# Optimization experiments

Measured on AMD Instinct MI355X. Metric: run time of the kernel, lower is better.

The kernel has to match this reference:

```python
import jax, jax.numpy as jnp
import numpy as np

# DH-SFNN: 2 dendritic LIF layers (denri, no tanh, reset-by-subtraction) + leaky readout integrator.
GAMMA = 0.5   # surrogate gradient scale
LENS = 0.5    # surrogate gradient width
VTH = 1.0     # spike threshold
DT = 1.0

@jax.custom_vjp
def spike_fn(x):
    # Heaviside forward, Gaussian surrogate backward (act_fun_adp)
    return (x > 0.0).astype(x.dtype)

def _spike_fwd(x):
    return spike_fn(x), x

def _spike_bwd(x, g):
    sg = GAMMA * jnp.exp(-x * x / (2.0 * LENS * LENS)) / (jnp.sqrt(2.0 * jnp.pi) * LENS)
    return (g * sg,)

spike_fn.defvjp(_spike_fwd, _spike_bwd)

B, T, IN, H, O, K = 256, 250, 700, 256, 20, 4  # batch, time, in_dim, hidden, out_dim, branch
WARMUP = 10


def _branch_mask(rng, out_dim, in_dim, k):
    # Each neuron's k branches see a disjoint random partition of the inputs.
    m = np.zeros((out_dim * k, in_dim), np.float32)
    step = in_dim // k
    for i in range(out_dim):
        perm = rng.permutation(in_dim)
        for j in range(k):
            m[i * k + j, perm[j * step:(j + 1) * step]] = 1.0
    return m


def setup_inputs() -> dict:
    key = jax.random.key(0)
    ks = jax.random.split(key, 12)
    rng = np.random.default_rng(0)
    s1 = 1.0 / np.sqrt(IN)
    s2 = 1.0 / np.sqrt(H)
    # branch-masked dense weights (apply_mask() already baked in)
    W1 = jax.random.uniform(ks[0], (H * K, IN), minval=-s1, maxval=s1) * jnp.asarray(_branch_mask(rng, H, IN, K))
    b1 = jax.random.uniform(ks[1], (H * K,), minval=-s1, maxval=s1)
    tau_n1 = jax.random.uniform(ks[2], (H, K), minval=2.0, maxval=6.0)
    tau_m1 = jax.random.uniform(ks[3], (H,), minval=0.0, maxval=4.0)
    W2 = jax.random.uniform(ks[4], (H * K, H), minval=-s2, maxval=s2) * jnp.asarray(_branch_mask(rng, H, H, K))
    b2 = jax.random.uniform(ks[5], (H * K,), minval=-s2, maxval=s2)
    tau_n2 = jax.random.uniform(ks[6], (H, K), minval=2.0, maxval=6.0)
    tau_m2 = jax.random.uniform(ks[7], (H,), minval=0.0, maxval=4.0)
    Wr = jax.random.uniform(ks[8], (O, H), minval=-s2, maxval=s2)
    br = jax.random.uniform(ks[9], (O,), minval=-s2, maxval=s2)
    tau_mr = jax.random.uniform(ks[10], (O,), minval=0.0, maxval=4.0)
    # sparse binary spike train input (SHD-like)
    x = (jax.random.uniform(ks[11], (B, T, IN)) < 0.1).astype(jnp.float32)
    return dict(x=x, W1=W1, b1=b1, tau_n1=tau_n1, tau_m1=tau_m1,
                W2=W2, b2=b2, tau_n2=tau_n2, tau_m2=tau_m2,
                Wr=Wr, br=br, tau_mr=tau_mr, warmup=WARMUP)


def reference(x, W1, b1, tau_n1, tau_m1, W2, b2, tau_n2, tau_m2, Wr, br, tau_mr, warmup):
    Bb, Tt, _ = x.shape
    beta1 = jax.nn.sigmoid(tau_n1)   # [H,K] dendritic decay
    alpha1 = jax.nn.sigmoid(tau_m1)  # [H]   soma decay
    beta2 = jax.nn.sigmoid(tau_n2)
    alpha2 = jax.nn.sigmoid(tau_m2)
    alphar = jax.nn.sigmoid(tau_mr)  # [O]

    def dense_branch(inp, W, b):
        return (inp @ W.T + b).reshape(inp.shape[0], -1, K)  # [B,H,K]

    def step(carry, xt):
        d1, m1, s1, d2, m2, s2, mr, acc, t = carry
        # layer 1: dendritic filtering then LIF with soft reset
        d1 = beta1 * d1 + (1.0 - beta1) * dense_branch(xt, W1, b1)
        m1 = m1 * alpha1 + (1.0 - alpha1) * DT * d1.sum(-1) - VTH * s1
        s1 = spike_fn(m1 - VTH)
        # layer 2
        d2 = beta2 * d2 + (1.0 - beta2) * dense_branch(s1, W2, b2)
        m2 = m2 * alpha2 + (1.0 - alpha2) * DT * d2.sum(-1) - VTH * s2
        s2 = spike_fn(m2 - VTH)
        # leaky readout integrator
        mr = mr * alphar + (1.0 - alphar) * (s2 @ Wr.T + br)
        acc = acc + jnp.where(t >= warmup, mr, jnp.zeros_like(mr))
        return (d1, m1, s1, d2, m2, s2, mr, acc, t + 1), None

    z = lambda *s: jnp.zeros(s, x.dtype)
    carry0 = (z(Bb, H, K), z(Bb, H), z(Bb, H),
              z(Bb, H, K), z(Bb, H), z(Bb, H),
              z(Bb, O), z(Bb, O), jnp.int32(0))
    carry, _ = jax.lax.scan(step, carry0, jnp.moveaxis(x, 1, 0))
    acc = carry[7]
    return acc / (Tt - warmup)  # readout_mode == 'mean'
```

## Files before the change

kernel.cpp:

```cpp
#include <hip/hip_runtime.h>
#include <hip/hip_bf16.h>

typedef unsigned short us16;
typedef unsigned int u32;

#define B_   256
#define T_   250
#define IN_  700
#define KP_  704
#define H_   256
#define O_   20
#define HK_  1024
#define NPAIR_ (B_ * T_)
#define LDP_ 40
#define CP_  136

typedef __attribute__((ext_vector_type(8))) short short8;
typedef __attribute__((ext_vector_type(4))) float f32x4;

__device__ __forceinline__ float bfbits(unsigned int lo16) {
    union { unsigned int i; float f; } v; v.i = lo16 << 16; return v.f;
}
__device__ __forceinline__ float bflo(unsigned int u) {
    union { unsigned int i; float f; } v; v.i = u << 16; return v.f;
}
__device__ __forceinline__ float bfhi(unsigned int u) {
    union { unsigned int i; float f; } v; v.i = u & 0xffff0000u; return v.f;
}
__device__ __forceinline__ us16 f2bfu(float f) {
    __hip_bfloat16 h = __float2bfloat16(f);
    union { __hip_bfloat16 h; us16 u; } c; c.h = h; return c.u;
}
__device__ __forceinline__ float sigm(float x) { return 1.0f / (1.0f + expf(-x)); }
__device__ __forceinline__ int rfl(int v) { return __builtin_amdgcn_readfirstlane(v); }

__device__ __forceinline__ bool detect_bf16(const us16* __restrict__ taun) {
    int ok = 0;
#pragma unroll
    for (int i = 0; i < 8; i += 2) ok += ((taun[i] >> 8) == 0x40) ? 1 : 0;
    return ok == 4;
}
__device__ __forceinline__ float ldany(const void* __restrict__ p, long i, bool isb) {
    return isb ? bfbits(((const us16*)p)[i]) : ((const float*)p)[i];
}

__device__ __forceinline__ void async_cp16(const us16* g, us16* l) {
    __builtin_amdgcn_global_load_lds(
        (const __attribute__((address_space(1))) u32*)g,
        (__attribute__((address_space(3))) u32*)l, 16, 0, 0);
}

__global__ __launch_bounds__(256) void cvt_rows2(
    const void* __restrict__ xin, const void* __restrict__ w1in,
    us16* __restrict__ xout, us16* __restrict__ w1out,
    const us16* __restrict__ taun) {
    const bool isb = detect_bf16(taun);
    const int r = blockIdx.x * 4 + (threadIdx.x >> 6);
    const int l = threadIdx.x & 63;
    const void* in; us16* out; long ibase, obase;
    if (r < NPAIR_) {
        in = xin;  out = xout;  ibase = (long)r * IN_; obase = (long)r * KP_;
    } else {
        const int r2 = r - NPAIR_;
        if (r2 >= HK_) return;
        in = w1in; out = w1out; ibase = (long)r2 * IN_; obase = (long)r2 * KP_;
    }
    for (int c = l; c < 88; c += 64) {
        uint4 o;
        if (c < 87) {
            if (isb) {
                uint2 lo = *(const uint2*)((const us16*)in + ibase + 8 * c);
                uint2 hi = *(const uint2*)((const us16*)in + ibase + 8 * c + 4);
                o.x = lo.x; o.y = lo.y; o.z = hi.x; o.w = hi.y;
            } else {
                float4 f0 = *(const float4*)((const float*)in + ibase + 8 * c);
                float4 f1 = *(const float4*)((const float*)in + ibase + 8 * c + 4);
                o.x = (u32)f2bfu(f0.x) | ((u32)f2bfu(f0.y) << 16);
                o.y = (u32)f2bfu(f0.z) | ((u32)f2bfu(f0.w) << 16);
                o.z = (u32)f2bfu(f1.x) | ((u32)f2bfu(f1.y) << 16);
                o.w = (u32)f2bfu(f1.z) | ((u32)f2bfu(f1.w) << 16);
            }
        } else {
            o.z = 0u; o.w = 0u;
            if (isb) {
                uint2 lo = *(const uint2*)((const us16*)in + ibase + 696);
                o.x = lo.x; o.y = lo.y;
            } else {
                float4 f0 = *(const float4*)((const float*)in + ibase + 696);
                o.x = (u32)f2bfu(f0.x) | ((u32)f2bfu(f0.y) << 16);
                o.y = (u32)f2bfu(f0.z) | ((u32)f2bfu(f0.w) << 16);
            }
        }
        *(uint4*)(out + obase + 8 * c) = o;
    }
}

__global__ void transpose_to_bf16(const void* __restrict__ in, us16* __restrict__ out,
                                  int R, int C, const us16* __restrict__ taun) {
    const bool isb = detect_bf16(taun);
    __shared__ us16 tile[32][33];
    int c0 = blockIdx.x * 32, r0 = blockIdx.y * 32;
    int tx = threadIdx.x, ty = threadIdx.y;
#pragma unroll
    for (int j = 0; j < 32; j += 8) {
        int r = r0 + ty + j, c = c0 + tx;
        if (r < R && c < C) tile[ty + j][tx] = f2bfu(ldany(in, (long)r * C + c, isb));
    }
    __syncthreads();
#pragma unroll
    for (int j = 0; j < 32; j += 8) {
        int c = c0 + ty + j, r = r0 + tx;
        if (c < C && r < R) out[(long)c * R + r] = tile[tx][ty + j];
    }
}

__global__ __launch_bounds__(256) void gemm_bf(
    const us16* __restrict__ Xb, const us16* __restrict__ W1b,
    us16* __restrict__ Apre)
{
    __shared__ __align__(16) us16 smem[32768];

    const int L  = blockIdx.x;
    const int mt = (L & 7) + ((L >> 6) << 3);
    const int nt = (L >> 3) & 7;
    if (mt >= NPAIR_ / 128) return;
    const int m0 = mt * 128, n0 = nt * 128;

    const int tid  = threadIdx.x;
    const int lane = tid & 63;
    const int w    = tid >> 6;
    const int wr   = w >> 1, wc = w & 1;
    const int l16  = lane & 15, quad = lane >> 4;

    const int rr    = lane >> 3;
    const int ccsw  = ((lane & 7) ^ rr) * 8;
    const us16* xg[4]; const us16* wg[4];
    int asl[4], bsl[4];
#pragma unroll
    for (int i = 0; i < 4; ++i) {
        const int blkrow = (w * 4 + i) * 8;
        xg[i]  = Xb  + (long)(m0 + blkrow + rr) * KP_ + ccsw;
        wg[i]  = W1b + (long)(n0 + blkrow + rr) * KP_ + ccsw;
        asl[i] = (w * 4 + i) * 512;
        bsl[i] = 8192 + (w * 4 + i) * 512;
    }

    f32x4 acc[4][4];
#pragma unroll
    for (int i = 0; i < 4; ++i)
#pragma unroll
        for (int j = 0; j < 4; ++j) acc[i][j] = (f32x4){0.f, 0.f, 0.f, 0.f};

    const int sw = l16 & 7;
    int aoff0[4], aoff1[4], boff0[4], boff1[4];
#pragma unroll
    for (int i = 0; i < 4; ++i) {
        const int ar = wr * 64 + i * 16 + l16;
        const int br = wc * 64 + i * 16 + l16;
        aoff0[i] = ar * 64 + ((quad ^ sw) << 3);
        aoff1[i] = ar * 64 + (((quad + 4) ^ sw) << 3);
        boff0[i] = 8192 + br * 64 + ((quad ^ sw) << 3);
        boff1[i] = 8192 + br * 64 + (((quad + 4) ^ sw) << 3);
    }

#pragma unroll
    for (int i = 0; i < 4; ++i) async_cp16(xg[i], smem + asl[i]);
#pragma unroll
    for (int i = 0; i < 4; ++i) async_cp16(wg[i], smem + bsl[i]);
    __syncthreads();

    for (int s = 0; s < 11; ++s) {
        const int cur = (s & 1) * 16384;
        const int nxt = 16384 - cur;
        if (s + 1 < 11) {
            const int kb = (s + 1) * 64;
#pragma unroll
            for (int i = 0; i < 4; ++i) async_cp16(xg[i] + kb, smem + nxt + asl[i]);
#pragma unroll
            for (int i = 0; i < 4; ++i) async_cp16(wg[i] + kb, smem + nxt + bsl[i]);
        }

        short8 af[4][2], bfv[4][2];
#pragma unroll
        for (int i = 0; i < 4; ++i) {
            af[i][0]  = *(const short8*)(smem + cur + aoff0[i]);
            af[i][1]  = *(const short8*)(smem + cur + aoff1[i]);
            bfv[i][0] = *(const short8*)(smem + cur + boff0[i]);
            bfv[i][1] = *(const short8*)(smem + cur + boff1[i]);
        }
#pragma unroll
        for (int h = 0; h < 2; ++h)
#pragma unroll
            for (int i = 0; i < 4; ++i)
#pragma unroll
                for (int j = 0; j < 4; ++j)
                    acc[i][j] = __builtin_amdgcn_mfma_f32_16x16x32_bf16(
                        af[i][h], bfv[j][h], acc[i][j], 0, 0, 0);

        __syncthreads();
    }

#pragma unroll
    for (int i = 0; i < 4; ++i)
#pragma unroll
        for (int j = 0; j < 4; ++j)
#pragma unroll
            for (int r = 0; r < 4; ++r)
                smem[(wr * 64 + i * 16 + quad * 4 + r) * CP_ +
                     (wc * 64 + j * 16 + l16)] = f2bfu(acc[i][j][r]);
    __syncthreads();
    {
        const int c8 = (lane & 15) * 8;
#pragma unroll
        for (int r2 = 0; r2 < 8; ++r2) {
            const int row = w * 32 + r2 * 4 + (lane >> 4);
            const uint4 v = *(const uint4*)(smem + row * CP_ + c8);
            *(uint4*)(Apre + (long)(m0 + row) * HK_ + n0 + c8) = v;
        }
    }
}

__global__ __launch_bounds__(64) void dhsfnn_wave2(
    const us16* __restrict__ Apre,
    const void* __restrict__ b1,  const void* __restrict__ tau_n1,
    const void* __restrict__ tau_m1,
    const void* __restrict__ b2,  const void* __restrict__ tau_n2,
    const void* __restrict__ tau_m2,
    const void* __restrict__ Wr,  const void* __restrict__ br,
    const void* __restrict__ tau_mr,
    const us16* __restrict__ W2T,
    const int* __restrict__ warmup_p,
    void* __restrict__ out)
{
    __shared__ __align__(16) us16 ring[2][16 * HK_];

    const int lane = threadIdx.x;
    const int b    = blockIdx.x;
    const bool isb = detect_bf16((const us16*)tau_n1);
    const int wu   = *warmup_p;

    const us16* apb = Apre + (long)b * T_ * HK_;

    for (int seg = 0; seg < 32; ++seg)
        async_cp16(apb + seg * 512 + lane * 8, ring[0] + seg * 512);

    float be1[16], cb1[16], ce1[16], be2[16], cb2[16], ce2[16], d1[16], d2[16];
#pragma unroll
    for (int e = 0; e < 16; ++e) {
        const long gi = (e < 8) ? ((long)lane * 8 + e) : (512 + (long)lane * 8 + e - 8);
        const float t1 = sigm(ldany(tau_n1, gi, isb));
        be1[e] = t1; ce1[e] = 1.f - t1; cb1[e] = ce1[e] * ldany(b1, gi, isb);
        const float t2 = sigm(ldany(tau_n2, gi, isb));
        be2[e] = t2; ce2[e] = 1.f - t2; cb2[e] = ce2[e] * ldany(b2, gi, isb);
        d1[e] = 0.f; d2[e] = 0.f;
    }
    float al1[4], cal1[4], al2[4], cal2[4], m1[4], s1[4], m2[4], s2[4];
#pragma unroll
    for (int j = 0; j < 4; ++j) {
        const int n = (j < 2) ? (2 * lane + j) : (128 + 2 * lane + (j - 2));
        al1[j] = sigm(ldany(tau_m1, n, isb)); cal1[j] = 1.f - al1[j];
        al2[j] = sigm(ldany(tau_m2, n, isb)); cal2[j] = 1.f - al2[j];
        m1[j] = 0.f; s1[j] = 0.f; m2[j] = 0.f; s2[j] = 0.f;
    }
    float alr = 0.f, brv = 0.f;
    if (lane < O_) { alr = sigm(ldany(tau_mr, lane, isb)); brv = ldany(br, lane, isb); }
    float mrv = 0.f, accO = 0.f;

    for (int c = 0; c < 16; ++c) {
        asm volatile("s_waitcnt vmcnt(0)" ::: "memory");

        if (c + 1 < 16) {
            const int t1c  = (c + 1) * 16;
            const int nseg = ((T_ - t1c < 16) ? (T_ - t1c) : 16) * 2;
            const us16* src = apb + (long)t1c * HK_;
            us16* dst = ring[(c + 1) & 1];
            for (int seg = 0; seg < nseg; ++seg)
                async_cp16(src + seg * 512 + lane * 8, dst + seg * 512);
        }

        const int t0 = c * 16;
        const int nst = (T_ - t0 < 16) ? (T_ - t0) : 16;
        const us16* rb = ring[c & 1];
        uint4 cLo = *(const uint4*)(rb + lane * 8);
        uint4 cHi = *(const uint4*)(rb + 512 + lane * 8);
        for (int q = 0; q < nst; ++q) {
            uint4 nLo = cLo, nHi = cHi;
            if (q + 1 < nst) {
                nLo = *(const uint4*)(rb + (q + 1) * HK_ + lane * 8);
                nHi = *(const uint4*)(rb + (q + 1) * HK_ + 512 + lane * 8);
            }
            const int t = t0 + q;
            float a[16];
            a[0]=bflo(cLo.x);  a[1]=bfhi(cLo.x);  a[2]=bflo(cLo.y);  a[3]=bfhi(cLo.y);
            a[4]=bflo(cLo.z);  a[5]=bfhi(cLo.z);  a[6]=bflo(cLo.w);  a[7]=bfhi(cLo.w);
            a[8]=bflo(cHi.x);  a[9]=bfhi(cHi.x);  a[10]=bflo(cHi.y); a[11]=bfhi(cHi.y);
            a[12]=bflo(cHi.z); a[13]=bfhi(cHi.z); a[14]=bflo(cHi.w); a[15]=bfhi(cHi.w);

#pragma unroll
            for (int e = 0; e < 16; ++e)
                d1[e] = be1[e] * d1[e] + cb1[e] + ce1[e] * a[e];

            unsigned long long bal1[4];
#pragma unroll
            for (int j = 0; j < 4; ++j) {
                const float s = (d1[j*4+0] + d1[j*4+1]) + (d1[j*4+2] + d1[j*4+3]);
                m1[j] = m1[j] * al1[j] + cal1[j] * s - s1[j];
                s1[j] = (m1[j] > 1.0f) ? 1.f : 0.f;
                bal1[j] = __ballot(s1[j] > 0.f);
            }

            if ((bal1[0] | bal1[1] | bal1[2] | bal1[3]) != 0ull) {
                float g[16];
#pragma unroll
                for (int e = 0; e < 16; ++e) g[e] = 0.f;
                for (int j2 = 0; j2 < 4; ++j2) {
                    unsigned long long mm = bal1[j2];
                    while (mm) {
                        const int i = __ffsll(mm) - 1; mm &= mm - 1;
                        const int n = (j2 < 2) ? (2 * i + j2) : (128 + 2 * i + (j2 - 2));
                        const us16* wv = W2T + ((long)n << 10);
                        const uint4 wl = *(const uint4*)(wv + lane * 8);
                        const uint4 wh = *(const uint4*)(wv + 512 + lane * 8);
                        g[0]+=bflo(wl.x);  g[1]+=bfhi(wl.x);  g[2]+=bflo(wl.y);  g[3]+=bfhi(wl.y);
                        g[4]+=bflo(wl.z);  g[5]+=bfhi(wl.z);  g[6]+=bflo(wl.w);  g[7]+=bfhi(wl.w);
                        g[8]+=bflo(wh.x);  g[9]+=bfhi(wh.x);  g[10]+=bflo(wh.y); g[11]+=bfhi(wh.y);
                        g[12]+=bflo(wh.z); g[13]+=bfhi(wh.z); g[14]+=bflo(wh.w); g[15]+=bfhi(wh.w);
                    }
                }
#pragma unroll
                for (int e = 0; e < 16; ++e)
                    d2[e] = be2[e] * d2[e] + cb2[e] + ce2[e] * g[e];
            } else {
#pragma unroll
                for (int e = 0; e < 16; ++e)
                    d2[e] = be2[e] * d2[e] + cb2[e];
            }

            unsigned long long bal2[4];
#pragma unroll
            for (int j = 0; j < 4; ++j) {
                const float s = (d2[j*4+0] + d2[j*4+1]) + (d2[j*4+2] + d2[j*4+3]);
                m2[j] = m2[j] * al2[j] + cal2[j] * s - s2[j];
                s2[j] = (m2[j] > 1.0f) ? 1.f : 0.f;
                bal2[j] = __ballot(s2[j] > 0.f);
            }

            if (lane < O_) {
                float sum = brv;
                if ((bal2[0] | bal2[1] | bal2[2] | bal2[3]) != 0ull) {
                    for (int j2 = 0; j2 < 4; ++j2) {
                        unsigned long long mm = bal2[j2];
                        while (mm) {
                            const int i = __ffsll(mm) - 1; mm &= mm - 1;
                            const int n = (j2 < 2) ? (2 * i + j2) : (128 + 2 * i + (j2 - 2));
                            sum += ldany(Wr, (long)lane * H_ + n, isb);
                        }
                    }
                }
                mrv = alr * mrv + (1.f - alr) * sum;
                if (t >= wu) accO += mrv;
            }
            cLo = nLo; cHi = nHi;
        }
    }

    if (lane < O_) {
        const float res = accO / (float)(T_ - wu);
        if (isb) ((us16*)out)[b * O_ + lane] = f2bfu(res);
        else     ((float*)out)[b * O_ + lane] = res;
    }
}

#define GA_LOAD(S, AV, BV) do {                                               \
    const int k0_ = (S) * 32 + half16;                                        \
    if (k0_ + 16 <= IN_) {                                                    \
        if (isb) {                                                            \
            const us16* pa_ = (const us16*)X  + arow + k0_;                   \
            const us16* pb_ = (const us16*)W1 + brow + k0_;                   \
            uint2 a0_ = *(const uint2*)pa_,        a1_ = *(const uint2*)(pa_ + 4);  \
            uint2 a2_ = *(const uint2*)(pa_ + 8),  a3_ = *(const uint2*)(pa_ + 12); \
            uint2 b0_ = *(const uint2*)pb_,        b1_ = *(const uint2*)(pb_ + 4);  \
            uint2 b2_ = *(const uint2*)(pb_ + 8),  b3_ = *(const uint2*)(pb_ + 12); \
            AV[0]=a0_.x; AV[1]=a0_.y; AV[2]=a1_.x; AV[3]=a1_.y;               \
            AV[4]=a2_.x; AV[5]=a2_.y; AV[6]=a3_.x; AV[7]=a3_.y;               \
            BV[0]=b0_.x; BV[1]=b0_.y; BV[2]=b1_.x; BV[3]=b1_.y;               \
            BV[4]=b2_.x; BV[5]=b2_.y; BV[6]=b3_.x; BV[7]=b3_.y;               \
        } else {                                                              \
            const float* pa_ = (const float*)X  + arow + k0_;                 \
            const float* pb_ = (const float*)W1 + brow + k0_;                 \
            float4 fa0_ = *(const float4*)pa_,        fa1_ = *(const float4*)(pa_ + 4);  \
            float4 fa2_ = *(const float4*)(pa_ + 8),  fa3_ = *(const float4*)(pa_ + 12); \
            float4 fb0_ = *(const float4*)pb_,        fb1_ = *(const float4*)(pb_ + 4);  \
            float4 fb2_ = *(const float4*)(pb_ + 8),  fb3_ = *(const float4*)(pb_ + 12); \
            AV[0] = (unsigned)f2bfu(fa0_.x) | ((unsigned)f2bfu(fa0_.y) << 16); \
            AV[1] = (unsigned)f2bfu(fa0_.z) | ((unsigned)f2bfu(fa0_.w) << 16); \
            AV[2] = (unsigned)f2bfu(fa1_.x) | ((unsigned)f2bfu(fa1_.y) << 16); \
            AV[3] = (unsigned)f2bfu(fa1_.z) | ((unsigned)f2bfu(fa1_.w) << 16); \
            AV[4] = (unsigned)f2bfu(fa2_.x) | ((unsigned)f2bfu(fa2_.y) << 16); \
            AV[5] = (unsigned)f2bfu(fa2_.z) | ((unsigned)f2bfu(fa2_.w) << 16); \
            AV[6] = (unsigned)f2bfu(fa3_.x) | ((unsigned)f2bfu(fa3_.y) << 16); \
            AV[7] = (unsigned)f2bfu(fa3_.z) | ((unsigned)f2bfu(fa3_.w) << 16); \
            BV[0] = (unsigned)f2bfu(fb0_.x) | ((unsigned)f2bfu(fb0_.y) << 16); \
            BV[1] = (unsigned)f2bfu(fb0_.z) | ((unsigned)f2bfu(fb0_.w) << 16); \
            BV[2] = (unsigned)f2bfu(fb1_.x) | ((unsigned)f2bfu(fb1_.y) << 16); \
            BV[3] = (unsigned)f2bfu(fb1_.z) | ((unsigned)f2bfu(fb1_.w) << 16); \
            BV[4] = (unsigned)f2bfu(fb2_.x) | ((unsigned)f2bfu(fb2_.y) << 16); \
            BV[5] = (unsigned)f2bfu(fb2_.z) | ((unsigned)f2bfu(fb2_.w) << 16); \
            BV[6] = (unsigned)f2bfu(fb3_.x) | ((unsigned)f2bfu(fb3_.y) << 16); \
            BV[7] = (unsigned)f2bfu(fb3_.z) | ((unsigned)f2bfu(fb3_.w) << 16); \
        }                                                                     \
    } else {                                                                  \
        _Pragma("unroll")                                                     \
        for (int e_ = 0; e_ < 8; ++e_) { AV[e_] = 0u; BV[e_] = 0u; }          \
        _Pragma("unroll")                                                     \
        for (int e_ = 0; e_ < 16; ++e_) {                                     \
            int k_ = k0_ + e_;                                                \
            if (k_ < IN_) {                                                   \
                unsigned va_ = (unsigned)f2bfu(ldany(X,  arow + k_, isb));    \
                unsigned vb_ = (unsigned)f2bfu(ldany(W1, brow + k_, isb));    \
                AV[e_ >> 1] |= va_ << ((e_ & 1) * 16);                        \
                BV[e_ >> 1] |= vb_ << ((e_ & 1) * 16);                        \
            }                                                                 \
        }                                                                     \
    }                                                                         \
} while (0)

#define GA_STORE(AV, BV) do {                                                 \
    uint4 u0_; u0_.x = AV[0]; u0_.y = AV[1]; u0_.z = AV[2]; u0_.w = AV[3];    \
    uint4 u1_; u1_.x = AV[4]; u1_.y = AV[5]; u1_.z = AV[6]; u1_.w = AV[7];    \
    uint4 v0_; v0_.x = BV[0]; v0_.y = BV[1]; v0_.z = BV[2]; v0_.w = BV[3];    \
    uint4 v1_; v1_.x = BV[4]; v1_.y = BV[5]; v1_.z = BV[6]; v1_.w = BV[7];    \
    *(uint4*)asw       = u0_; *(uint4*)(asw + 8) = u1_;                       \
    *(uint4*)bsw       = v0_; *(uint4*)(bsw + 8) = v1_;                       \
} while (0)

#define GA_MFMA() do {                                                        \
    short8 af_[4], bf_[4];                                                    \
    _Pragma("unroll")                                                         \
    for (int i_ = 0; i_ < 4; ++i_) af_[i_] = *(const short8*)(As + aoff[i_]); \
    _Pragma("unroll")                                                         \
    for (int j_ = 0; j_ < 4; ++j_) bf_[j_] = *(const short8*)(Bs + boff[j_]); \
    _Pragma("unroll")                                                         \
    for (int i_ = 0; i_ < 4; ++i_)                                            \
        _Pragma("unroll")                                                     \
        for (int j_ = 0; j_ < 4; ++j_)                                        \
            acc[i_][j_] = __builtin_amdgcn_mfma_f32_16x16x32_bf16(            \
                af_[i_], bf_[j_], acc[i_][j_], 0, 0, 0);                      \
} while (0)

__global__ __launch_bounds__(256) void gemm_apre(
    const void* __restrict__ X, const void* __restrict__ W1,
    const us16* __restrict__ taun, us16* __restrict__ Apre)
{
    const bool isb = detect_bf16(taun);
    __shared__ __align__(16) us16 As[128 * LDP_];
    __shared__ __align__(16) us16 Bs[128 * LDP_];

    const int L  = blockIdx.x;
    const int mt = (L & 7) + ((L >> 6) << 3);
    const int nt = (L >> 3) & 7;
    if (mt >= NPAIR_ / 128) return;
    const int m0 = mt * 128, n0 = nt * 128;

    const int tid  = threadIdx.x;
    const int lane = tid & 63;
    const int w    = tid >> 6;
    const int wr   = w >> 1, wc = w & 1;
    const int l16  = lane & 15, quad = lane >> 4;
    const int ra   = tid >> 1;
    const int half16 = (tid & 1) * 16;

    f32x4 acc[4][4];
#pragma unroll
    for (int i = 0; i < 4; ++i)
#pragma unroll
        for (int j = 0; j < 4; ++j) acc[i][j] = (f32x4){0.f, 0.f, 0.f, 0.f};

    int aoff[4], boff[4];
#pragma unroll
    for (int i = 0; i < 4; ++i) {
        aoff[i] = (wr * 64 + i * 16 + l16) * LDP_ + quad * 8;
        boff[i] = (wc * 64 + i * 16 + l16) * LDP_ + quad * 8;
    }

    const long arow = (long)(m0 + ra) * IN_;
    const long brow = (long)(n0 + ra) * IN_;
    us16* asw = As + ra * LDP_ + half16;
    us16* bsw = Bs + ra * LDP_ + half16;

    unsigned av0[8], bv0[8], av1[8], bv1[8];
    GA_LOAD(0, av0, bv0);

    for (int ss = 0; ss < 11; ++ss) {
        __syncthreads();
        GA_STORE(av0, bv0);
        __syncthreads();
        GA_LOAD(2 * ss + 1, av1, bv1);
        GA_MFMA();
        __syncthreads();
        GA_STORE(av1, bv1);
        __syncthreads();
        if (ss < 10) GA_LOAD(2 * ss + 2, av0, bv0);
        GA_MFMA();
    }

#pragma unroll
    for (int i = 0; i < 4; ++i) {
#pragma unroll
        for (int j = 0; j < 4; ++j) {
            const int gm = m0 + wr * 64 + i * 16 + quad * 4;
            const int gn = n0 + wc * 64 + j * 16 + l16;
            us16* op = Apre + (long)gm * HK_ + gn;
#pragma unroll
            for (int r = 0; r < 4; ++r)
                op[(long)r * HK_] = f2bfu(acc[i][j][r]);
        }
    }
}

__global__ __launch_bounds__(64) void dhsfnn_wave(
    const us16* __restrict__ Apre,
    const void* __restrict__ b1,  const void* __restrict__ tau_n1,
    const void* __restrict__ tau_m1,
    const void* __restrict__ b2,  const void* __restrict__ tau_n2,
    const void* __restrict__ tau_m2,
    const void* __restrict__ Wr,  const void* __restrict__ br,
    const void* __restrict__ tau_mr,
    const us16* __restrict__ W2T,
    const int* __restrict__ warmup_p,
    void* __restrict__ out)
{
    const int lane = threadIdx.x;
    const int b    = blockIdx.x;
    const bool isb = detect_bf16((const us16*)tau_n1);
    const int wu   = *warmup_p;

    float be1[16], cb1[16], be2[16], cb2[16], d1[16], d2[16];
#pragma unroll
    for (int e = 0; e < 16; ++e) {
        const long gi = (long)lane * 16 + e;
        const float t1 = sigm(ldany(tau_n1, gi, isb));
        be1[e] = t1; cb1[e] = (1.f - t1) * ldany(b1, gi, isb);
        const float t2 = sigm(ldany(tau_n2, gi, isb));
        be2[e] = t2; cb2[e] = (1.f - t2) * ldany(b2, gi, isb);
        d1[e] = 0.f; d2[e] = 0.f;
    }
    float al1[4], al2[4], m1[4], s1[4], m2[4], s2[4];
#pragma unroll
    for (int j = 0; j < 4; ++j) {
        al1[j] = sigm(ldany(tau_m1, lane * 4 + j, isb));
        al2[j] = sigm(ldany(tau_m2, lane * 4 + j, isb));
        m1[j] = 0.f; s1[j] = 0.f; m2[j] = 0.f; s2[j] = 0.f;
    }
    float alr = 0.f, brv = 0.f;
    if (lane < O_) { alr = sigm(ldany(tau_mr, lane, isb)); brv = ldany(br, lane, isb); }
    float mrv = 0.f, accO = 0.f;

    const us16* ap = Apre + (long)b * T_ * HK_ + lane * 16;

    auto wstep = [&](int t, uint4 lo, uint4 hi) {
        float a[16];
        a[0]=bflo(lo.x);  a[1]=bfhi(lo.x);  a[2]=bflo(lo.y);  a[3]=bfhi(lo.y);
        a[4]=bflo(lo.z);  a[5]=bfhi(lo.z);  a[6]=bflo(lo.w);  a[7]=bfhi(lo.w);
        a[8]=bflo(hi.x);  a[9]=bfhi(hi.x);  a[10]=bflo(hi.y); a[11]=bfhi(hi.y);
        a[12]=bflo(hi.z); a[13]=bfhi(hi.z); a[14]=bflo(hi.w); a[15]=bfhi(hi.w);
#pragma unroll
        for (int e = 0; e < 16; ++e)
            d1[e] = be1[e] * d1[e] + cb1[e] + (1.f - be1[e]) * a[e];
        unsigned long long bal1[4];
#pragma unroll
        for (int j = 0; j < 4; ++j) {
            const float s = (d1[j*4+0] + d1[j*4+1]) + (d1[j*4+2] + d1[j*4+3]);
            m1[j] = m1[j] * al1[j] + (1.f - al1[j]) * s - s1[j];
            s1[j] = (m1[j] > 1.0f) ? 1.f : 0.f;
            bal1[j] = __ballot(s1[j] > 0.f);
        }
        if ((bal1[0] | bal1[1] | bal1[2] | bal1[3]) != 0ull) {
            float g[16];
#pragma unroll
            for (int e = 0; e < 16; ++e) g[e] = 0.f;
            for (int j2 = 0; j2 < 4; ++j2) {
                unsigned long long mm = bal1[j2];
                while (mm) {
                    const int i = __ffsll(mm) - 1; mm &= mm - 1;
                    const us16* wv = W2T + ((long)(i * 4 + j2) << 10) + lane * 16;
                    const uint4 wl = *(const uint4*)wv;
                    const uint4 wh = *(const uint4*)(wv + 8);
                    g[0]+=bflo(wl.x);  g[1]+=bfhi(wl.x);  g[2]+=bflo(wl.y);  g[3]+=bfhi(wl.y);
                    g[4]+=bflo(wl.z);  g[5]+=bfhi(wl.z);  g[6]+=bflo(wl.w);  g[7]+=bfhi(wl.w);
                    g[8]+=bflo(wh.x);  g[9]+=bfhi(wh.x);  g[10]+=bflo(wh.y); g[11]+=bfhi(wh.y);
                    g[12]+=bflo(wh.z); g[13]+=bfhi(wh.z); g[14]+=bflo(wh.w); g[15]+=bfhi(wh.w);
                }
            }
#pragma unroll
            for (int e = 0; e < 16; ++e)
                d2[e] = be2[e] * d2[e] + cb2[e] + (1.f - be2[e]) * g[e];
        } else {
#pragma unroll
            for (int e = 0; e < 16; ++e)
                d2[e] = be2[e] * d2[e] + cb2[e];
        }
        unsigned long long bal2[4];
#pragma unroll
        for (int j = 0; j < 4; ++j) {
            const float s = (d2[j*4+0] + d2[j*4+1]) + (d2[j*4+2] + d2[j*4+3]);
            m2[j] = m2[j] * al2[j] + (1.f - al2[j]) * s - s2[j];
            s2[j] = (m2[j] > 1.0f) ? 1.f : 0.f;
            bal2[j] = __ballot(s2[j] > 0.f);
        }
        if (lane < O_) {
            float sum = brv;
            if ((bal2[0] | bal2[1] | bal2[2] | bal2[3]) != 0ull) {
                for (int j2 = 0; j2 < 4; ++j2) {
                    unsigned long long mm = bal2[j2];
                    while (mm) {
                        const int i = __ffsll(mm) - 1; mm &= mm - 1;
                        sum += ldany(Wr, (long)lane * H_ + (i * 4 + j2), isb);
                    }
                }
            }
            mrv = alr * mrv + (1.f - alr) * sum;
            if (t >= wu) accO += mrv;
        }
    };

    uint4 q0a = *(const uint4*)(ap);
    uint4 q0b = *(const uint4*)(ap + 8);
    uint4 q1a = *(const uint4*)(ap + HK_);
    uint4 q1b = *(const uint4*)(ap + HK_ + 8);
    uint4 q2a = *(const uint4*)(ap + 2 * HK_);
    uint4 q2b = *(const uint4*)(ap + 2 * HK_ + 8);
    uint4 q3a = *(const uint4*)(ap + 3 * HK_);
    uint4 q3b = *(const uint4*)(ap + 3 * HK_ + 8);

    int t = 0;
    for (int it = 0; it < 62; ++it) {
        wstep(t + 0, q0a, q0b);
        q0a = *(const uint4*)(ap + (long)(t + 4) * HK_);
        q0b = *(const uint4*)(ap + (long)(t + 4) * HK_ + 8);
        wstep(t + 1, q1a, q1b);
        if (t + 5 < T_) {
            q1a = *(const uint4*)(ap + (long)(t + 5) * HK_);
            q1b = *(const uint4*)(ap + (long)(t + 5) * HK_ + 8);
        }
        wstep(t + 2, q2a, q2b);
        if (t + 6 < T_) {
            q2a = *(const uint4*)(ap + (long)(t + 6) * HK_);
            q2b = *(const uint4*)(ap + (long)(t + 6) * HK_ + 8);
        }
        wstep(t + 3, q3a, q3b);
        if (t + 7 < T_) {
            q3a = *(const uint4*)(ap + (long)(t + 7) * HK_);
            q3b = *(const uint4*)(ap + (long)(t + 7) * HK_ + 8);
        }
        t += 4;
    }
    wstep(248, q0a, q0b);
    wstep(249, q1a, q1b);

    if (lane < O_) {
        const float res = accO / (float)(T_ - wu);
        if (isb) ((us16*)out)[b * O_ + lane] = f2bfu(res);
        else     ((float*)out)[b * O_ + lane] = res;
    }
}

__global__ __launch_bounds__(256) void dhsfnn_fb(
    const void* __restrict__ x,  const void* __restrict__ W1,
    const void* __restrict__ b1, const void* __restrict__ tau_n1,
    const void* __restrict__ tau_m1,
    const void* __restrict__ W2, const void* __restrict__ b2,
    const void* __restrict__ tau_n2, const void* __restrict__ tau_m2,
    const void* __restrict__ Wr, const void* __restrict__ br,
    const void* __restrict__ tau_mr,
    const int* __restrict__ warmup_p,
    void* __restrict__ out)
{
    __shared__ us16 list1[1024];
    __shared__ us16 list2[256];
    __shared__ us16 list3[256];
    __shared__ int n1s, n2s, n3s;

    const int tid = threadIdx.x;
    const int b   = blockIdx.x;
    const int h   = tid;
    const bool isb = detect_bf16((const us16*)tau_n1);
    const int wu  = *warmup_p;

    const float be1_0 = sigm(ldany(tau_n1, 4 * h + 0, isb));
    const float be1_1 = sigm(ldany(tau_n1, 4 * h + 1, isb));
    const float be1_2 = sigm(ldany(tau_n1, 4 * h + 2, isb));
    const float be1_3 = sigm(ldany(tau_n1, 4 * h + 3, isb));
    const float bi1_0 = ldany(b1, 4 * h + 0, isb), bi1_1 = ldany(b1, 4 * h + 1, isb);
    const float bi1_2 = ldany(b1, 4 * h + 2, isb), bi1_3 = ldany(b1, 4 * h + 3, isb);
    const float al1 = sigm(ldany(tau_m1, h, isb));
    const float be2_0 = sigm(ldany(tau_n2, 4 * h + 0, isb));
    const float be2_1 = sigm(ldany(tau_n2, 4 * h + 1, isb));
    const float be2_2 = sigm(ldany(tau_n2, 4 * h + 2, isb));
    const float be2_3 = sigm(ldany(tau_n2, 4 * h + 3, isb));
    const float bi2_0 = ldany(b2, 4 * h + 0, isb), bi2_1 = ldany(b2, 4 * h + 1, isb);
    const float bi2_2 = ldany(b2, 4 * h + 2, isb), bi2_3 = ldany(b2, 4 * h + 3, isb);
    const float al2 = sigm(ldany(tau_m2, h, isb));
    float alr = 0.f, brv = 0.f;
    if (h < O_) { alr = sigm(ldany(tau_mr, h, isb)); brv = ldany(br, h, isb); }

    float d1_0 = 0.f, d1_1 = 0.f, d1_2 = 0.f, d1_3 = 0.f, m1v = 0.f, s1f = 0.f;
    float d2_0 = 0.f, d2_1 = 0.f, d2_2 = 0.f, d2_3 = 0.f, m2v = 0.f, s2f = 0.f;
    float mrv = 0.f, accO = 0.f;

    const long xbase = (long)b * T_ * IN_;
    float xv0 = ldany(x, xbase + tid, isb);
    float xv1 = ldany(x, xbase + tid + 256, isb);
    float xv2 = (tid + 512 < IN_) ? ldany(x, xbase + tid + 512, isb) : 0.f;

    for (int t = 0; t < T_; ++t) {
        const bool p0 = xv0 != 0.f, p1 = xv1 != 0.f, p2 = xv2 != 0.f;
        if (t + 1 < T_) {
            const long nbx = xbase + (long)(t + 1) * IN_;
            xv0 = ldany(x, nbx + tid, isb);
            xv1 = ldany(x, nbx + tid + 256, isb);
            xv2 = (tid + 512 < IN_) ? ldany(x, nbx + tid + 512, isb) : 0.f;
        }
        __syncthreads();
        if (tid == 0) { n1s = 0; n2s = 0; n3s = 0; }
        __syncthreads();
        if (p0) { int p = atomicAdd(&n1s, 1); list1[p & 1023] = (us16)tid; }
        if (p1) { int p = atomicAdd(&n1s, 1); list1[p & 1023] = (us16)(tid + 256); }
        if (p2) { int p = atomicAdd(&n1s, 1); list1[p & 1023] = (us16)(tid + 512); }
        __syncthreads();
        int n1 = n1s; n1 = (n1 < 1024) ? n1 : 1024;

        float a0 = 0.f, a1 = 0.f, a2 = 0.f, a3 = 0.f;
#pragma unroll 2
        for (int idx = 0; idx < n1; ++idx) {
            int i = rfl((int)list1[idx]);
            i = (i < IN_) ? i : (IN_ - 1);
            long r = (long)(h * 4) * IN_ + i;
            a0 += ldany(W1, r, isb);
            a1 += ldany(W1, r + IN_, isb);
            a2 += ldany(W1, r + 2 * IN_, isb);
            a3 += ldany(W1, r + 3 * IN_, isb);
        }
        d1_0 = be1_0 * d1_0 + (1.f - be1_0) * (bi1_0 + a0);
        d1_1 = be1_1 * d1_1 + (1.f - be1_1) * (bi1_1 + a1);
        d1_2 = be1_2 * d1_2 + (1.f - be1_2) * (bi1_2 + a2);
        d1_3 = be1_3 * d1_3 + (1.f - be1_3) * (bi1_3 + a3);
        m1v = m1v * al1 + (1.f - al1) * (d1_0 + d1_1 + d1_2 + d1_3) - s1f;
        s1f = (m1v > 1.0f) ? 1.f : 0.f;

        if (s1f > 0.f) { int p = atomicAdd(&n2s, 1); list2[p & 255] = (us16)tid; }
        __syncthreads();
        int n2 = n2s; n2 = (n2 < 256) ? n2 : 256;

        a0 = 0.f; a1 = 0.f; a2 = 0.f; a3 = 0.f;
#pragma unroll 2
        for (int idx = 0; idx < n2; ++idx) {
            int i = rfl((int)list2[idx]);
            i = (i < H_) ? i : (H_ - 1);
            long r = (long)(h * 4) * H_ + i;
            a0 += ldany(W2, r, isb);
            a1 += ldany(W2, r + H_, isb);
            a2 += ldany(W2, r + 2 * H_, isb);
            a3 += ldany(W2, r + 3 * H_, isb);
        }
        d2_0 = be2_0 * d2_0 + (1.f - be2_0) * (bi2_0 + a0);
        d2_1 = be2_1 * d2_1 + (1.f - be2_1) * (bi2_1 + a1);
        d2_2 = be2_2 * d2_2 + (1.f - be2_2) * (bi2_2 + a2);
        d2_3 = be2_3 * d2_3 + (1.f - be2_3) * (bi2_3 + a3);
        m2v = m2v * al2 + (1.f - al2) * (d2_0 + d2_1 + d2_2 + d2_3) - s2f;
        s2f = (m2v > 1.0f) ? 1.f : 0.f;

        if (s2f > 0.f) { int p = atomicAdd(&n3s, 1); list3[p & 255] = (us16)tid; }
        __syncthreads();
        int n3 = n3s; n3 = (n3 < 256) ? n3 : 256;

        if (h < O_) {
            float sum = brv;
            for (int idx = 0; idx < n3; ++idx) {
                int j = (int)list3[idx];
                j = (j < H_) ? j : (H_ - 1);
                sum += ldany(Wr, (long)h * H_ + j, isb);
            }
            mrv = alr * mrv + (1.f - alr) * sum;
            if (t >= wu) accO += mrv;
        }
    }
    if (h < O_) {
        float res = accO / (float)(T_ - wu);
        if (isb) ((us16*)out)[b * O_ + h] = f2bfu(res);
        else     ((float*)out)[b * O_ + h] = res;
    }
}

extern "C" void kernel_launch(void* const* d_in, const int* in_sizes, int n_in,
                              void* d_out, int out_size, void* d_ws, size_t ws_size,
                              hipStream_t stream) {
    const void* x      = d_in[0];
    const void* W1     = d_in[1];
    const void* b1     = d_in[2];
    const void* tau_n1 = d_in[3];
    const void* tau_m1 = d_in[4];
    const void* W2     = d_in[5];
    const void* b2     = d_in[6];
    const void* tau_n2 = d_in[7];
    const void* tau_m2 = d_in[8];
    const void* Wr     = d_in[9];
    const void* br     = d_in[10];
    const void* tau_mr = d_in[11];
    const int*  warmup = (const int*)d_in[12];

    const size_t w2t_bytes  = (size_t)H_ * HK_ * 2;
    const size_t xbf_bytes  = (size_t)NPAIR_ * KP_ * 2;
    const size_t w1b_bytes  = (size_t)HK_ * KP_ * 2;
    const size_t apre_bytes = (size_t)NPAIR_ * HK_ * 2;

    const bool tier0 = (d_ws != nullptr &&
                        ws_size >= w2t_bytes + xbf_bytes + w1b_bytes + apre_bytes);
    const bool tier1 = (d_ws != nullptr && ws_size >= w2t_bytes + apre_bytes);

    dim3 blk(32, 8);
    if (tier0) {
        us16* W2T  = (us16*)d_ws;
        us16* Xbf  = (us16*)((char*)d_ws + w2t_bytes);
        us16* W1bf = (us16*)((char*)d_ws + w2t_bytes + xbf_bytes);
        us16* Apre = (us16*)((char*)d_ws + w2t_bytes + xbf_bytes + w1b_bytes);
        cvt_rows2<<<(NPAIR_ + HK_) / 4, 256, 0, stream>>>(
            x, W1, Xbf, W1bf, (const us16*)tau_n1);
        transpose_to_bf16<<<dim3((H_ + 31) / 32, (HK_ + 31) / 32), blk, 0, stream>>>(
            W2, W2T, HK_, H_, (const us16*)tau_n1);
        gemm_bf<<<4096, 256, 0, stream>>>(Xbf, W1bf, Apre);
        dhsfnn_wave2<<<B_, 64, 0, stream>>>(
            Apre, b1, tau_n1, tau_m1, b2, tau_n2, tau_m2,
            Wr, br, tau_mr, W2T, warmup, d_out);
    } else if (tier1) {
        us16* W2T  = (us16*)d_ws;
        us16* Apre = (us16*)((char*)d_ws + w2t_bytes);
        transpose_to_bf16<<<dim3((H_ + 31) / 32, (HK_ + 31) / 32), blk, 0, stream>>>(
            W2, W2T, HK_, H_, (const us16*)tau_n1);
        gemm_apre<<<4096, 256, 0, stream>>>(x, W1, (const us16*)tau_n1, Apre);
        dhsfnn_wave<<<B_, 64, 0, stream>>>(
            Apre, b1, tau_n1, tau_m1, b2, tau_n2, tau_m2,
            Wr, br, tau_mr, W2T, warmup, d_out);
    } else {
        dhsfnn_fb<<<B_, 256, 0, stream>>>(x, W1, b1, tau_n1, tau_m1,
                                          W2, b2, tau_n2, tau_m2,
                                          Wr, br, tau_mr, warmup, d_out);
    }
}
```

Before: 468.2 us.

## Split recurrent scan across four waves with LDS spike-mask exchange and layer skew

Replaces the single-wave-per-batch recurrent kernel with a 256-thread block where each thread owns one hidden neuron and its 4 branches. Spike ballots are exchanged through small double-buffered LDS masks, and layer 1 of step t+1 is computed alongside layer 2 of step t so that only one barrier is needed per timestep. The LDS ring buffer of async copies is dropped in favour of direct register prefetch of Apre four steps ahead. This shortens the serial per-step dependency chain and increases parallelism, at the cost of a block barrier every timestep and smaller per-thread memory loads.

```diff
diff --git a/kernel.cpp b/kernel.cpp
--- a/kernel.cpp
+++ b/kernel.cpp
@@ -3,6 +3,7 @@
 
 typedef unsigned short us16;
 typedef unsigned int u32;
+typedef unsigned long long ull;
 
 #define B_   256
 #define T_   250
@@ -49,6 +50,10 @@
         (const __attribute__((address_space(1))) u32*)g,
         (__attribute__((address_space(3))) u32*)l, 16, 0, 0);
 }
+
+#define BAR_LDS() do {                                                   \
+    asm volatile("s_waitcnt lgkmcnt(0)\n\ts_barrier" ::: "memory");      \
+} while (0)
 
 __global__ __launch_bounds__(256) void cvt_rows2(
     const void* __restrict__ xin, const void* __restrict__ w1in,
@@ -220,7 +225,7 @@
     }
 }
 
-__global__ __launch_bounds__(64) void dhsfnn_wave2(
+__global__ __launch_bounds__(256) void dhsfnn_4w(
     const us16* __restrict__ Apre,
     const void* __restrict__ b1,  const void* __restrict__ tau_n1,
     const void* __restrict__ tau_m1,
@@ -232,142 +237,135 @@
     const int* __restrict__ warmup_p,
     void* __restrict__ out)
 {
-    __shared__ __align__(16) us16 ring[2][16 * HK_];
-
-    const int lane = threadIdx.x;
+    __shared__ ull msk1[2][4];
+    __shared__ ull msk2[2][4];
+
+    const int tid  = threadIdx.x;
+    const int lane = tid & 63;
+    const int w    = tid >> 6;
     const int b    = blockIdx.x;
     const bool isb = detect_bf16((const us16*)tau_n1);
     const int wu   = *warmup_p;
 
-    const us16* apb = Apre + (long)b * T_ * HK_;
-
-    for (int seg = 0; seg < 32; ++seg)
-        async_cp16(apb + seg * 512 + lane * 8, ring[0] + seg * 512);
-
-    float be1[16], cb1[16], ce1[16], be2[16], cb2[16], ce2[16], d1[16], d2[16];
-#pragma unroll
-    for (int e = 0; e < 16; ++e) {
-        const long gi = (e < 8) ? ((long)lane * 8 + e) : (512 + (long)lane * 8 + e - 8);
+    float be1[4], cb1[4], ce1[4], be2[4], cb2[4], ce2[4], d1[4], d2[4];
+#pragma unroll
+    for (int k = 0; k < 4; ++k) {
+        const long gi = 4L * tid + k;
         const float t1 = sigm(ldany(tau_n1, gi, isb));
-        be1[e] = t1; ce1[e] = 1.f - t1; cb1[e] = ce1[e] * ldany(b1, gi, isb);
+        be1[k] = t1; ce1[k] = 1.f - t1; cb1[k] = ce1[k] * ldany(b1, gi, isb);
         const float t2 = sigm(ldany(tau_n2, gi, isb));
-        be2[e] = t2; ce2[e] = 1.f - t2; cb2[e] = ce2[e] * ldany(b2, gi, isb);
-        d1[e] = 0.f; d2[e] = 0.f;
-    }
-    float al1[4], cal1[4], al2[4], cal2[4], m1[4], s1[4], m2[4], s2[4];
-#pragma unroll
-    for (int j = 0; j < 4; ++j) {
-        const int n = (j < 2) ? (2 * lane + j) : (128 + 2 * lane + (j - 2));
-        al1[j] = sigm(ldany(tau_m1, n, isb)); cal1[j] = 1.f - al1[j];
-        al2[j] = sigm(ldany(tau_m2, n, isb)); cal2[j] = 1.f - al2[j];
-        m1[j] = 0.f; s1[j] = 0.f; m2[j] = 0.f; s2[j] = 0.f;
-    }
+        be2[k] = t2; ce2[k] = 1.f - t2; cb2[k] = ce2[k] * ldany(b2, gi, isb);
+        d1[k] = 0.f; d2[k] = 0.f;
+    }
+    const float al1 = sigm(ldany(tau_m1, tid, isb)), cal1 = 1.f - al1;
+    const float al2 = sigm(ldany(tau_m2, tid, isb)), cal2 = 1.f - al2;
+    float m1 = 0.f, s1f = 0.f, m2 = 0.f, s2f = 0.f;
     float alr = 0.f, brv = 0.f;
-    if (lane < O_) { alr = sigm(ldany(tau_mr, lane, isb)); brv = ldany(br, lane, isb); }
+    if (tid < O_) { alr = sigm(ldany(tau_mr, tid, isb)); brv = ldany(br, tid, isb); }
     float mrv = 0.f, accO = 0.f;
 
-    for (int c = 0; c < 16; ++c) {
-        asm volatile("s_waitcnt vmcnt(0)" ::: "memory");
-
-        if (c + 1 < 16) {
-            const int t1c  = (c + 1) * 16;
-            const int nseg = ((T_ - t1c < 16) ? (T_ - t1c) : 16) * 2;
-            const us16* src = apb + (long)t1c * HK_;
-            us16* dst = ring[(c + 1) & 1];
-            for (int seg = 0; seg < nseg; ++seg)
-                async_cp16(src + seg * 512 + lane * 8, dst + seg * 512);
-        }
-
-        const int t0 = c * 16;
-        const int nst = (T_ - t0 < 16) ? (T_ - t0) : 16;
-        const us16* rb = ring[c & 1];
-        uint4 cLo = *(const uint4*)(rb + lane * 8);
-        uint4 cHi = *(const uint4*)(rb + 512 + lane * 8);
-        for (int q = 0; q < nst; ++q) {
-            uint4 nLo = cLo, nHi = cHi;
-            if (q + 1 < nst) {
-                nLo = *(const uint4*)(rb + (q + 1) * HK_ + lane * 8);
-                nHi = *(const uint4*)(rb + (q + 1) * HK_ + 512 + lane * 8);
+    const us16* ap = Apre + (long)b * T_ * HK_ + 4 * tid;
+
+    uint2 q0 = *(const uint2*)(ap);
+    uint2 q1 = *(const uint2*)(ap + HK_);
+    uint2 q2 = *(const uint2*)(ap + 2 * HK_);
+    uint2 q3 = *(const uint2*)(ap + 3 * HK_);
+
+    {
+        const float a0 = bflo(q0.x), a1 = bfhi(q0.x), a2 = bflo(q0.y), a3 = bfhi(q0.y);
+        d1[0] = be1[0] * d1[0] + cb1[0] + ce1[0] * a0;
+        d1[1] = be1[1] * d1[1] + cb1[1] + ce1[1] * a1;
+        d1[2] = be1[2] * d1[2] + cb1[2] + ce1[2] * a2;
+        d1[3] = be1[3] * d1[3] + cb1[3] + ce1[3] * a3;
+        const float s = (d1[0] + d1[1]) + (d1[2] + d1[3]);
+        m1 = m1 * al1 + cal1 * s - s1f;
+        s1f = (m1 > 1.0f) ? 1.f : 0.f;
+        const ull bm = __ballot(s1f > 0.f);
+        if (lane == 0) msk1[0][w] = bm;
+    }
+    BAR_LDS();
+
+    auto body = [&](int t, uint2& q, bool doL1) {
+        const ull p0 = msk1[t & 1][0], p1 = msk1[t & 1][1];
+        const ull p2 = msk1[t & 1][2], p3 = msk1[t & 1][3];
+        d2[0] = be2[0] * d2[0] + cb2[0];
+        d2[1] = be2[1] * d2[1] + cb2[1];
+        d2[2] = be2[2] * d2[2] + cb2[2];
+        d2[3] = be2[3] * d2[3] + cb2[3];
+        if ((p0 | p1 | p2 | p3) != 0ull) {
+            float g0 = 0.f, g1 = 0.f, g2 = 0.f, g3 = 0.f;
+#pragma unroll
+            for (int w2 = 0; w2 < 4; ++w2) {
+                ull mm = (w2 == 0) ? p0 : (w2 == 1) ? p1 : (w2 == 2) ? p2 : p3;
+                while (mm) {
+                    const int i = __ffsll(mm) - 1; mm &= mm - 1;
+                    const int n = 64 * w2 + i;
+                    const uint2 wv = *(const uint2*)(W2T + ((long)n << 10) + 4 * tid);
+                    g0 += bflo(wv.x); g1 += bfhi(wv.x);
+                    g2 += bflo(wv.y); g3 += bfhi(wv.y);
+                }
             }
-            const int t = t0 + q;
-            float a[16];
-            a[0]=bflo(cLo.x);  a[1]=bfhi(cLo.x);  a[2]=bflo(cLo.y);  a[3]=bfhi(cLo.y);
-            a[4]=bflo(cLo.z);  a[5]=bfhi(cLo.z);  a[6]=bflo(cLo.w);  a[7]=bfhi(cLo.w);
-            a[8]=bflo(cHi.x);  a[9]=bfhi(cHi.x);  a[10]=bflo(cHi.y); a[11]=bfhi(cHi.y);
-            a[12]=bflo(cHi.z); a[13]=bfhi(cHi.z); a[14]=bflo(cHi.w); a[15]=bfhi(cHi.w);
-
-#pragma unroll
-            for (int e = 0; e < 16; ++e)
-                d1[e] = be1[e] * d1[e] + cb1[e] + ce1[e] * a[e];
-
-            unsigned long long bal1[4];
-#pragma unroll
-            for (int j = 0; j < 4; ++j) {
-                const float s = (d1[j*4+0] + d1[j*4+1]) + (d1[j*4+2] + d1[j*4+3]);
-                m1[j] = m1[j] * al1[j] + cal1[j] * s - s1[j];
-                s1[j] = (m1[j] > 1.0f) ? 1.f : 0.f;
-                bal1[j] = __ballot(s1[j] > 0.f);
-            }
-
-            if ((bal1[0] | bal1[1] | bal1[2] | bal1[3]) != 0ull) {
-                float g[16];
-#pragma unroll
-                for (int e = 0; e < 16; ++e) g[e] = 0.f;
-                for (int j2 = 0; j2 < 4; ++j2) {
-                    unsigned long long mm = bal1[j2];
-                    while (mm) {
-                        const int i = __ffsll(mm) - 1; mm &= mm - 1;
-                        const int n = (j2 < 2) ? (2 * i + j2) : (128 + 2 * i + (j2 - 2));
-                        const us16* wv = W2T + ((long)n << 10);
-                        const uint4 wl = *(const uint4*)(wv + lane * 8);
-                        const uint4 wh = *(const uint4*)(wv + 512 + lane * 8);
-                        g[0]+=bflo(wl.x);  g[1]+=bfhi(wl.x);  g[2]+=bflo(wl.y);  g[3]+=bfhi(wl.y);
-                        g[4]+=bflo(wl.z);  g[5]+=bfhi(wl.z);  g[6]+=bflo(wl.w);  g[7]+=bfhi(wl.w);
-                        g[8]+=bflo(wh.x);  g[9]+=bfhi(wh.x);  g[10]+=bflo(wh.y); g[11]+=bfhi(wh.y);
-                        g[12]+=bflo(wh.z); g[13]+=bfhi(wh.z); g[14]+=bflo(wh.w); g[15]+=bfhi(wh.w);
-                    }
-                }
-#pragma unroll
-                for (int e = 0; e < 16; ++e)
-                    d2[e] = be2[e] * d2[e] + cb2[e] + ce2[e] * g[e];
-            } else {
-#pragma unroll
-                for (int e = 0; e < 16; ++e)
-                    d2[e] = be2[e] * d2[e] + cb2[e];
-            }
-
-            unsigned long long bal2[4];
-#pragma unroll
-            for (int j = 0; j < 4; ++j) {
-                const float s = (d2[j*4+0] + d2[j*4+1]) + (d2[j*4+2] + d2[j*4+3]);
-                m2[j] = m2[j] * al2[j] + cal2[j] * s - s2[j];
-                s2[j] = (m2[j] > 1.0f) ? 1.f : 0.f;
-                bal2[j] = __ballot(s2[j] > 0.f);
-            }
-
+            d2[0] += ce2[0] * g0; d2[1] += ce2[1] * g1;
+            d2[2] += ce2[2] * g2; d2[3] += ce2[3] * g3;
+        }
+        const float s2s = (d2[0] + d2[1]) + (d2[2] + d2[3]);
+        m2 = m2 * al2 + cal2 * s2s - s2f;
+        s2f = (m2 > 1.0f) ? 1.f : 0.f;
+        const ull b2m = __ballot(s2f > 0.f);
+        if (lane == 0) msk2[t & 1][w] = b2m;
+
+        if (doL1) {
+            const float a0 = bflo(q.x), a1 = bfhi(q.x), a2 = bflo(q.y), a3 = bfhi(q.y);
+            if (t + 5 < T_) q = *(const uint2*)(ap + (long)(t + 5) * HK_);
+            d1[0] = be1[0] * d1[0] + cb1[0] + ce1[0] * a0;
+            d1[1] = be1[1] * d1[1] + cb1[1] + ce1[1] * a1;
+            d1[2] = be1[2] * d1[2] + cb1[2] + ce1[2] * a2;
+            d1[3] = be1[3] * d1[3] + cb1[3] + ce1[3] * a3;
+            const float s = (d1[0] + d1[1]) + (d1[2] + d1[3]);
+            m1 = m1 * al1 + cal1 * s - s1f;
+            s1f = (m1 > 1.0f) ? 1.f : 0.f;
+            const ull b1m = __ballot(s1f > 0.f);
+            if (lane == 0) msk1[(t + 1) & 1][w] = b1m;
+        }
+
+        BAR_LDS();
+
+        if (w == 0) {
+            const ull r0 = msk2[t & 1][0], r1 = msk2[t & 1][1];
+            const ull r2 = msk2[t & 1][2], r3 = msk2[t & 1][3];
             if (lane < O_) {
                 float sum = brv;
-                if ((bal2[0] | bal2[1] | bal2[2] | bal2[3]) != 0ull) {
-                    for (int j2 = 0; j2 < 4; ++j2) {
-                        unsigned long long mm = bal2[j2];
+                if ((r0 | r1 | r2 | r3) != 0ull) {
+#pragma unroll
+                    for (int w2 = 0; w2 < 4; ++w2) {
+                        ull mm = (w2 == 0) ? r0 : (w2 == 1) ? r1 : (w2 == 2) ? r2 : r3;
                         while (mm) {
                             const int i = __ffsll(mm) - 1; mm &= mm - 1;
-                            const int n = (j2 < 2) ? (2 * i + j2) : (128 + 2 * i + (j2 - 2));
-                            sum += ldany(Wr, (long)lane * H_ + n, isb);
+                            sum += ldany(Wr, (long)lane * H_ + 64 * w2 + i, isb);
                         }
                     }
                 }
                 mrv = alr * mrv + (1.f - alr) * sum;
                 if (t >= wu) accO += mrv;
             }
-            cLo = nLo; cHi = nHi;
-        }
-    }
-
-    if (lane < O_) {
+        }
+    };
+
+    int t = 0;
+    for (int it = 0; it < 62; ++it) {
+        body(t + 0, q1, true);
+        body(t + 1, q2, true);
+        body(t + 2, q3, true);
+        body(t + 3, q0, true);
+        t += 4;
+    }
+    body(248, q1, true);
+    body(249, q2, false);
+
+    if (tid < O_) {
         const float res = accO / (float)(T_ - wu);
-        if (isb) ((us16*)out)[b * O_ + lane] = f2bfu(res);
-        else     ((float*)out)[b * O_ + lane] = res;
+        if (isb) ((us16*)out)[b * O_ + tid] = f2bfu(res);
+        else     ((float*)out)[b * O_ + tid] = res;
     }
 }
 
@@ -829,7 +827,7 @@
         transpose_to_bf16<<<dim3((H_ + 31) / 32, (HK_ + 31) / 32), blk, 0, stream>>>(
             W2, W2T, HK_, H_, (const us16*)tau_n1);
         gemm_bf<<<4096, 256, 0, stream>>>(Xbf, W1bf, Apre);
-        dhsfnn_wave2<<<B_, 64, 0, stream>>>(
+        dhsfnn_4w<<<B_, 256, 0, stream>>>(
             Apre, b1, tau_n1, tau_m1, b2, tau_n2, tau_m2,
             Wr, br, tau_mr, W2T, warmup, d_out);
     } else if (tier1) {
```

Result: faster. 456.1 us (-2.6%).
